# Optimization experiments

Hardware: AMD Instinct MI355X
Metric: run time of the kernel (lower is better)

Reference implementation:

```python
import jax, jax.numpy as jnp
import numpy as np

N_USERS = 100000
N_ITEMS = 50000
N = N_USERS + N_ITEMS
NNZ = 2400000
D = 64
L = 3
B = 16384


def setup_inputs() -> dict:
    key = jax.random.key(0)
    ks = jax.random.split(key, 12)
    return {
        "user_emb": jax.random.normal(ks[0], (N_USERS, D), jnp.float32) * 0.1,
        "item_emb": jax.random.normal(ks[1], (N_ITEMS, D), jnp.float32) * 0.1,
        "W_gc": jax.random.normal(ks[2], (L, D, D), jnp.float32) * 0.1,
        "b_gc": jax.random.normal(ks[3], (L, 1, D), jnp.float32) * 0.1,
        "W_bi": jax.random.normal(ks[4], (L, D, D), jnp.float32) * 0.1,
        "b_bi": jax.random.normal(ks[5], (L, 1, D), jnp.float32) * 0.1,
        "adj_vals": jax.random.uniform(ks[6], (NNZ,), jnp.float32) * (1.0 / 16.0),
        "adj_rows": jax.random.randint(ks[7], (NNZ,), 0, N, jnp.int32),
        "adj_cols": jax.random.randint(ks[8], (NNZ,), 0, N, jnp.int32),
        "u": jax.random.randint(ks[9], (B,), 0, N_USERS, jnp.int32),
        "i": jax.random.randint(ks[10], (B,), 0, N_ITEMS, jnp.int32),
        "j": jax.random.randint(ks[11], (B,), 0, N_ITEMS, jnp.int32),
    }


def reference(user_emb, item_emb, W_gc, b_gc, W_bi, b_bi, adj_vals, adj_rows, adj_cols, u, i, j):
    n_users = user_emb.shape[0]
    n_nodes = n_users + item_emb.shape[0]
    ego = jnp.concatenate([user_emb, item_emb], axis=0)  # [N, D]
    all_emb = [ego]
    n_layers = W_gc.shape[0]
    for l in range(n_layers):
        # spmm: side = A_hat @ ego  (edge-list gather + weighted segment sum)
        gathered = ego[adj_cols] * adj_vals[:, None]            # [nnz, D]
        side = jax.ops.segment_sum(gathered, adj_rows, num_segments=n_nodes)  # [N, D]
        # graph-conv branch
        sum_emb = jax.nn.leaky_relu(side @ W_gc[l] + b_gc[l], 0.2)
        # bi-interaction branch
        bi_emb = jax.nn.leaky_relu((ego * side) @ W_bi[l] + b_bi[l], 0.2)
        ego = sum_emb + bi_emb
        # L2 normalize per node (F.normalize, eps=1e-12)
        norm = ego / jnp.maximum(jnp.linalg.norm(ego, axis=1, keepdims=True), 1e-12)
        all_emb.append(norm)
    final = jnp.concatenate(all_emb, axis=1)  # [N, D*(L+1)]
    u_g = final[u]
    i_g = final[n_users + i]
    j_g = final[n_users + j]
    return u_g, i_g, j_g
```

## Files before the change

kernel.cpp:

```cpp
#include <hip/hip_runtime.h>

#define DD 64
#define RB 256
#define RB_SHIFT 8
#define CAP 4608
#define NBLKA 512
#define NBLKA_SHIFT 9
#define BMAX 1024
#define COLM 0x3FFFF
#define OVFCAP 65536
#define WT_STRIDE 80
#define EMAX 4704

typedef __attribute__((ext_vector_type(8))) short bf16x8;
typedef __attribute__((ext_vector_type(4))) float f32x4;

static __device__ __forceinline__ float leaky(float x) {
    return x > 0.f ? x : 0.2f * x;
}

static __device__ __forceinline__ unsigned short f2bf(float f) {
    unsigned u = __float_as_uint(f);
    unsigned r = 0x7FFFu + ((u >> 16) & 1u);
    return (unsigned short)((u + r) >> 16);
}
#define BF_LO(w) __int_as_float((int)((w) << 16))
#define BF_HI(w) __int_as_float((int)((w) & 0xFFFF0000u))

static __device__ __forceinline__ bf16x8 pack8(float a, float b, float c, float d,
                                               float e, float f, float g, float h) {
    bf16x8 r;
    r[0] = (short)f2bf(a); r[1] = (short)f2bf(b); r[2] = (short)f2bf(c); r[3] = (short)f2bf(d);
    r[4] = (short)f2bf(e); r[5] = (short)f2bf(f); r[6] = (short)f2bf(g); r[7] = (short)f2bf(h);
    return r;
}

__global__ void concat_kernel(const float4* __restrict__ ue, const float4* __restrict__ ie,
                              float4* __restrict__ ego, ushort4* __restrict__ egob,
                              int n_user4, int total4) {
    int idx = blockIdx.x * blockDim.x + threadIdx.x;
    if (idx >= total4) return;
    float4 v = (idx < n_user4) ? ue[idx] : ie[idx - n_user4];
    ego[idx] = v;
    ushort4 b;
    b.x = f2bf(v.x); b.y = f2bf(v.y); b.z = f2bf(v.z); b.w = f2bf(v.w);
    egob[idx] = b;
}

__global__ void bhist_kernel(const int* __restrict__ rows, int* __restrict__ counts_t, int nnz,
                             int nbuckets) {
    __shared__ int h[BMAX];
    int tid = threadIdx.x, blk = blockIdx.x;
    for (int i = tid; i < nbuckets; i += 256) h[i] = 0;
    __syncthreads();
    int chunk = (nnz + NBLKA - 1) / NBLKA;
    int lo = blk * chunk, hi = min(nnz, lo + chunk);
    for (int e = lo + tid; e < hi; e += 256) atomicAdd(&h[rows[e] >> RB_SHIFT], 1);
    __syncthreads();
    for (int i = tid; i < nbuckets; i += 256) counts_t[blk * nbuckets + i] = h[i];
}

__global__ void scan1_kernel(const int* __restrict__ counts_t, int* __restrict__ offsets,
                             int* __restrict__ blocksums, int flat, int nbuckets) {
    __shared__ int tmp[1024];
    int t = threadIdx.x;
    int g = blockIdx.x * 1024 + t;
    int x = 0;
    if (g < flat) {
        int i = g >> NBLKA_SHIFT, blk = g & (NBLKA - 1);
        x = counts_t[blk * nbuckets + i];
    }
    tmp[t] = x;
    __syncthreads();
    for (int off = 1; off < 1024; off <<= 1) {
        int y = (t >= off) ? tmp[t - off] : 0;
        __syncthreads();
        tmp[t] += y;
        __syncthreads();
    }
    if (g < flat) offsets[g + 1] = tmp[t];
    if (t == 1023) blocksums[blockIdx.x] = tmp[t];
    if (g == 0) offsets[0] = 0;
}

__global__ void scan2_kernel(int* blocksums, int nb) {
    __shared__ int tmp[1024];
    int t = threadIdx.x;
    int v = (t < nb) ? blocksums[t] : 0;
    tmp[t] = v;
    __syncthreads();
    for (int off = 1; off < 1024; off <<= 1) {
        int y = (t >= off) ? tmp[t - off] : 0;
        __syncthreads();
        tmp[t] += y;
        __syncthreads();
    }
    if (t < nb) blocksums[t] = tmp[t] - v;
}

__global__ void scan3_kernel(int* __restrict__ offsets, const int* __restrict__ blocksums,
                             int n) {
    int g = blockIdx.x * 1024 + threadIdx.x;
    if (g < n) offsets[g + 1] += blocksums[blockIdx.x];
}

__global__ void __launch_bounds__(256) bscatter_kernel(
    const int* __restrict__ rows, const int* __restrict__ cols,
    const float* __restrict__ vals, const int* __restrict__ offsets,
    int2* __restrict__ csr_cv, int nnz, int nbuckets) {
    __shared__ int hist[BMAX];
    __shared__ int lbase[BMAX];
    __shared__ int cur[BMAX];
    __shared__ int gcur[BMAX];
    __shared__ int tsum[256];
    __shared__ int2 buf[EMAX];
    __shared__ int dst[EMAX];
    int tid = threadIdx.x, blk = blockIdx.x;
    int chunk = (nnz + NBLKA - 1) / NBLKA;
    int lo = blk * chunk, hi = min(nnz, lo + chunk);
    for (int i = tid; i < BMAX; i += 256)
        gcur[i] = (i < nbuckets) ? offsets[i * NBLKA + blk] : 0;
    for (int sub = lo; sub < hi; sub += EMAX) {
        int scount = min(EMAX, hi - sub);
        for (int i = tid; i < BMAX; i += 256) hist[i] = 0;
        __syncthreads();
        for (int e = sub + tid; e < sub + scount; e += 256)
            atomicAdd(&hist[rows[e] >> RB_SHIFT], 1);
        __syncthreads();
        int loc[4];
        int s = 0;
        int bi = tid * 4;
#pragma unroll
        for (int j = 0; j < 4; ++j) { loc[j] = s; s += hist[bi + j]; }
        tsum[tid] = s;
        __syncthreads();
        for (int off = 1; off < 256; off <<= 1) {
            int v = (tid >= off) ? tsum[tid - off] : 0;
            __syncthreads();
            tsum[tid] += v;
            __syncthreads();
        }
        int excl = tid ? tsum[tid - 1] : 0;
#pragma unroll
        for (int j = 0; j < 4; ++j) {
            lbase[bi + j] = excl + loc[j];
            cur[bi + j] = excl + loc[j];
        }
        __syncthreads();
        for (int e = sub + tid; e < sub + scount; e += 256) {
            int r = rows[e];
            int b = r >> RB_SHIFT;
            int p = atomicAdd(&cur[b], 1);
            int2 cv;
            cv.x = ((r & (RB - 1)) << 18) | cols[e];
            cv.y = __float_as_int(vals[e]);
            buf[p] = cv;
            dst[p] = gcur[b] + (p - lbase[b]);
        }
        __syncthreads();
        for (int k = tid; k < scount; k += 256) csr_cv[dst[k]] = buf[k];
        __syncthreads();
        for (int i = tid; i < BMAX; i += 256) gcur[i] += hist[i];
        __syncthreads();
    }
}

__global__ void __launch_bounds__(256) sort_kernel(
    const int* __restrict__ offsets, const int2* __restrict__ csr_cv,
    int2* __restrict__ sorted_cv, int* __restrict__ rowoff_g,
    int4* __restrict__ ovf, int* __restrict__ ovf_cnt, int nnz, int nbuckets) {
    __shared__ int2 sorted[CAP];
    __shared__ int hist[RB];
    __shared__ int rowoff[RB + 1];
    __shared__ int cur[RB];
    int tid = threadIdx.x;
    int b = blockIdx.x;
    int s = offsets[b * NBLKA];
    int e = offsets[(b + 1) * NBLKA];
    int m = min(e - s, CAP);

    hist[tid] = 0;
    __syncthreads();
    for (int k = s + tid; k < s + m; k += 256)
        atomicAdd(&hist[((unsigned)csr_cv[k].x) >> 18], 1);
    __syncthreads();
    for (int off = 1; off < RB; off <<= 1) {
        int v = (tid >= off) ? hist[tid - off] : 0;
        __syncthreads();
        hist[tid] += v;
        __syncthreads();
    }
    rowoff[tid + 1] = hist[tid];
    if (tid == 0) rowoff[0] = 0;
    __syncthreads();
    cur[tid] = rowoff[tid];
    __syncthreads();
    for (int k = s + tid; k < s + m; k += 256) {
        int2 cv = csr_cv[k];
        int p = atomicAdd(&cur[((unsigned)cv.x) >> 18], 1);
        sorted[p] = cv;
    }
    __syncthreads();
    for (int k = tid; k < m; k += 256) sorted_cv[s + k] = sorted[k];
    rowoff_g[b * RB + tid] = s + rowoff[tid];
    if (b == 0 && tid == 0) rowoff_g[nbuckets * RB] = nnz;
    for (int k = s + CAP + tid; k < e; k += 256) {
        int2 cv = csr_cv[k];
        int p = atomicAdd(ovf_cnt, 1);
        if (p < OVFCAP) {
            int4 o;
            o.x = b * RB + (int)(((unsigned)cv.x) >> 18);
            o.y = cv.x & COLM;
            o.z = cv.y;
            o.w = 0;
            ovf[p] = o;
        }
    }
}

__global__ void spmm_csr_kernel(const uint4* __restrict__ egob4,
                                const int* __restrict__ rowoff,
                                const int2* __restrict__ sorted_cv,
                                float4* __restrict__ side4, int n) {
    int wid = (blockIdx.x * blockDim.x + threadIdx.x) >> 6;
    int lane = threadIdx.x & 63;
    int sub = lane >> 3, l8 = lane & 7;
    int row = wid * 8 + sub;
    if (row >= n) return;
    int s = rowoff[row], e = rowoff[row + 1];
    float acc[8] = {0.f, 0.f, 0.f, 0.f, 0.f, 0.f, 0.f, 0.f};
    int k = s;
    for (; k + 4 <= e; k += 4) {
        int2 c0 = sorted_cv[k];
        int2 c1 = sorted_cv[k + 1];
        int2 c2 = sorted_cv[k + 2];
        int2 c3 = sorted_cv[k + 3];
        uint4 g0 = egob4[(c0.x & COLM) * 8 + l8];
        uint4 g1 = egob4[(c1.x & COLM) * 8 + l8];
        uint4 g2 = egob4[(c2.x & COLM) * 8 + l8];
        uint4 g3 = egob4[(c3.x & COLM) * 8 + l8];
        float v0 = __int_as_float(c0.y), v1 = __int_as_float(c1.y);
        float v2 = __int_as_float(c2.y), v3 = __int_as_float(c3.y);
        acc[0] += v0 * BF_LO(g0.x); acc[1] += v0 * BF_HI(g0.x);
        acc[2] += v0 * BF_LO(g0.y); acc[3] += v0 * BF_HI(g0.y);
        acc[4] += v0 * BF_LO(g0.z); acc[5] += v0 * BF_HI(g0.z);
        acc[6] += v0 * BF_LO(g0.w); acc[7] += v0 * BF_HI(g0.w);
        acc[0] += v1 * BF_LO(g1.x); acc[1] += v1 * BF_HI(g1.x);
        acc[2] += v1 * BF_LO(g1.y); acc[3] += v1 * BF_HI(g1.y);
        acc[4] += v1 * BF_LO(g1.z); acc[5] += v1 * BF_HI(g1.z);
        acc[6] += v1 * BF_LO(g1.w); acc[7] += v1 * BF_HI(g1.w);
        acc[0] += v2 * BF_LO(g2.x); acc[1] += v2 * BF_HI(g2.x);
        acc[2] += v2 * BF_LO(g2.y); acc[3] += v2 * BF_HI(g2.y);
        acc[4] += v2 * BF_LO(g2.z); acc[5] += v2 * BF_HI(g2.z);
        acc[6] += v2 * BF_LO(g2.w); acc[7] += v2 * BF_HI(g2.w);
        acc[0] += v3 * BF_LO(g3.x); acc[1] += v3 * BF_HI(g3.x);
        acc[2] += v3 * BF_LO(g3.y); acc[3] += v3 * BF_HI(g3.y);
        acc[4] += v3 * BF_LO(g3.z); acc[5] += v3 * BF_HI(g3.z);
        acc[6] += v3 * BF_LO(g3.w); acc[7] += v3 * BF_HI(g3.w);
    }
    for (; k < e; ++k) {
        int2 cv = sorted_cv[k];
        uint4 g = egob4[(cv.x & COLM) * 8 + l8];
        float v = __int_as_float(cv.y);
        acc[0] += v * BF_LO(g.x); acc[1] += v * BF_HI(g.x);
        acc[2] += v * BF_LO(g.y); acc[3] += v * BF_HI(g.y);
        acc[4] += v * BF_LO(g.z); acc[5] += v * BF_HI(g.z);
        acc[6] += v * BF_LO(g.w); acc[7] += v * BF_HI(g.w);
    }
    float4 o0 = {acc[0], acc[1], acc[2], acc[3]};
    float4 o1 = {acc[4], acc[5], acc[6], acc[7]};
    side4[row * 16 + l8 * 2] = o0;
    side4[row * 16 + l8 * 2 + 1] = o1;
}

__global__ void ovf_fix_kernel(const int4* __restrict__ ovf, const int* __restrict__ ovf_cnt,
                               const float* __restrict__ ego, float* __restrict__ side) {
    int total = min(*ovf_cnt, OVFCAP);
    for (int i = blockIdx.x * blockDim.x + threadIdx.x; i < total * DD;
         i += gridDim.x * blockDim.x) {
        int e = i >> 6, d = i & 63;
        int4 o = ovf[e];
        atomicAdd(&side[o.x * DD + d], __int_as_float(o.z) * ego[o.y * DD + d]);
    }
}

__global__ void __launch_bounds__(256) transform_kernel(
    const float* __restrict__ side, float* __restrict__ ego, ushort* __restrict__ egob,
    const float* __restrict__ Wgc, const float* __restrict__ bgc,
    const float* __restrict__ Wbi, const float* __restrict__ bbi, int n) {
    __shared__ __align__(16) ushort sWg[DD * WT_STRIDE];
    __shared__ __align__(16) ushort sWb[DD * WT_STRIDE];
    int tid = threadIdx.x;
    for (int idx = tid; idx < DD * DD; idx += 256) {
        int k = idx >> 6, c = idx & 63;
        sWg[c * WT_STRIDE + k] = f2bf(Wgc[idx]);
        sWb[c * WT_STRIDE + k] = f2bf(Wbi[idx]);
    }
    __syncthreads();

    int wave = tid >> 6, lane = tid & 63;
    int ntiles = (n + 15) >> 4;
    int tile = blockIdx.x * 4 + wave;
    if (tile >= ntiles) return;
    int base = tile * 16;
    int m = lane & 15, quad = lane >> 4;
    int row = base + m;
    if (row >= n) row = n - 1;

    const float4* srow = (const float4*)(side + (size_t)row * DD);
    const float4* erow = (const float4*)(ego + (size_t)row * DD);
    float4 s0 = srow[quad * 2], s1 = srow[quad * 2 + 1];
    float4 s2 = srow[8 + quad * 2], s3 = srow[8 + quad * 2 + 1];
    float4 e0 = erow[quad * 2], e1 = erow[quad * 2 + 1];
    float4 e2 = erow[8 + quad * 2], e3 = erow[8 + quad * 2 + 1];

    bf16x8 aS_lo = pack8(s0.x, s0.y, s0.z, s0.w, s1.x, s1.y, s1.z, s1.w);
    bf16x8 aS_hi = pack8(s2.x, s2.y, s2.z, s2.w, s3.x, s3.y, s3.z, s3.w);
    bf16x8 aP_lo = pack8(e0.x * s0.x, e0.y * s0.y, e0.z * s0.z, e0.w * s0.w,
                         e1.x * s1.x, e1.y * s1.y, e1.z * s1.z, e1.w * s1.w);
    bf16x8 aP_hi = pack8(e2.x * s2.x, e2.y * s2.y, e2.z * s2.z, e2.w * s2.w,
                         e3.x * s3.x, e3.y * s3.y, e3.z * s3.z, e3.w * s3.w);

    f32x4 accG[4], accB[4];
#pragma unroll
    for (int ct = 0; ct < 4; ++ct) {
        accG[ct] = (f32x4){0.f, 0.f, 0.f, 0.f};
        accB[ct] = (f32x4){0.f, 0.f, 0.f, 0.f};
    }
#pragma unroll
    for (int ct = 0; ct < 4; ++ct) {
        int col = ct * 16 + m;
        bf16x8 bg_lo = *(const bf16x8*)&sWg[col * WT_STRIDE + quad * 8];
        bf16x8 bg_hi = *(const bf16x8*)&sWg[col * WT_STRIDE + 32 + quad * 8];
        bf16x8 bb_lo = *(const bf16x8*)&sWb[col * WT_STRIDE + quad * 8];
        bf16x8 bb_hi = *(const bf16x8*)&sWb[col * WT_STRIDE + 32 + quad * 8];
        accG[ct] = __builtin_amdgcn_mfma_f32_16x16x32_bf16(aS_lo, bg_lo, accG[ct], 0, 0, 0);
        accG[ct] = __builtin_amdgcn_mfma_f32_16x16x32_bf16(aS_hi, bg_hi, accG[ct], 0, 0, 0);
        accB[ct] = __builtin_amdgcn_mfma_f32_16x16x32_bf16(aP_lo, bb_lo, accB[ct], 0, 0, 0);
        accB[ct] = __builtin_amdgcn_mfma_f32_16x16x32_bf16(aP_hi, bb_hi, accB[ct], 0, 0, 0);
    }

#pragma unroll
    for (int ct = 0; ct < 4; ++ct) {
        int col = ct * 16 + m;
        float bg = bgc[col], bb = bbi[col];
#pragma unroll
        for (int r = 0; r < 4; ++r) {
            int node = base + quad * 4 + r;
            if (node < n) {
                float o = leaky(accG[ct][r] + bg) + leaky(accB[ct][r] + bb);
                ego[(size_t)node * DD + col] = o;
                egob[(size_t)node * DD + col] = f2bf(o);
            }
        }
    }
}

__global__ void gather_kernel(const float* __restrict__ ego, const int* __restrict__ u,
                              const int* __restrict__ ii, const int* __restrict__ jj,
                              float* __restrict__ out, int layer, int B, int n_users,
                              int normalize) {
    int wid = (blockIdx.x * blockDim.x + threadIdx.x) >> 6;
    int lane = threadIdx.x & 63;
    if (wid >= 3 * B) return;
    int arr = wid / B;
    int b = wid - arr * B;
    int node = (arr == 0) ? u[b] : ((arr == 1) ? n_users + ii[b] : n_users + jj[b]);
    float v = ego[node * DD + lane];
    if (normalize) {
        float ss = v * v;
#pragma unroll
        for (int m = 32; m; m >>= 1) ss += __shfl_xor(ss, m, 64);
        v /= fmaxf(sqrtf(ss), 1e-12f);
    }
    out[wid * 256 + layer * DD + lane] = v;
}

extern "C" void kernel_launch(void* const* d_in, const int* in_sizes, int n_in,
                              void* d_out, int out_size, void* d_ws, size_t ws_size,
                              hipStream_t stream) {
    const float* user_emb = (const float*)d_in[0];
    const float* item_emb = (const float*)d_in[1];
    const float* W_gc = (const float*)d_in[2];
    const float* b_gc = (const float*)d_in[3];
    const float* W_bi = (const float*)d_in[4];
    const float* b_bi = (const float*)d_in[5];
    const float* adj_vals = (const float*)d_in[6];
    const int* adj_rows = (const int*)d_in[7];
    const int* adj_cols = (const int*)d_in[8];
    const int* u = (const int*)d_in[9];
    const int* ii = (const int*)d_in[10];
    const int* jj = (const int*)d_in[11];
    float* out = (float*)d_out;

    const int D = DD;
    int n_users = in_sizes[0] / D;
    int n_items = in_sizes[1] / D;
    int n = n_users + n_items;
    int nnz = in_sizes[6];
    int B = in_sizes[9];
    int L = in_sizes[2] / (D * D);

    int nbuckets = (n + RB - 1) / RB;
    int flat = nbuckets * NBLKA;

    char* ws = (char*)d_ws;
    auto alloc = [&](size_t bytes) {
        char* p = ws;
        ws += (bytes + 255) & ~(size_t)255;
        return p;
    };
    float* ego = (float*)alloc((size_t)n * D * 4);
    ushort* egob = (ushort*)alloc((size_t)n * D * 2);
    float* side = (float*)alloc((size_t)n * D * 4);
    int* counts_t = (int*)alloc((size_t)flat * 4);
    int* offsets = (int*)alloc((size_t)(flat + 1) * 4);
    int* blocksums = (int*)alloc(4096);
    int2* csr_cv = (int2*)alloc((size_t)nnz * 8);
    int2* sorted_cv = (int2*)alloc((size_t)nnz * 8);
    int* rowoff = (int*)alloc((size_t)(nbuckets * RB + 1) * 4);
    int4* ovf = (int4*)alloc((size_t)OVFCAP * 16);
    int* ovf_cnt = (int*)alloc(256);

    int total4 = n * D / 4, nu4 = n_users * D / 4;
    concat_kernel<<<(total4 + 255) / 256, 256, 0, stream>>>(
        (const float4*)user_emb, (const float4*)item_emb, (float4*)ego, (ushort4*)egob,
        nu4, total4);

    int grows = 3 * B;
    gather_kernel<<<(grows + 3) / 4, 256, 0, stream>>>(ego, u, ii, jj, out, 0, B, n_users, 0);

    hipMemsetAsync(ovf_cnt, 0, 4, stream);
    bhist_kernel<<<NBLKA, 256, 0, stream>>>(adj_rows, counts_t, nnz, nbuckets);
    int nblk1 = (flat + 1023) / 1024;
    scan1_kernel<<<nblk1, 1024, 0, stream>>>(counts_t, offsets, blocksums, flat, nbuckets);
    scan2_kernel<<<1, 1024, 0, stream>>>(blocksums, nblk1);
    scan3_kernel<<<nblk1, 1024, 0, stream>>>(offsets, blocksums, flat);
    bscatter_kernel<<<NBLKA, 256, 0, stream>>>(adj_rows, adj_cols, adj_vals, offsets, csr_cv,
                                               nnz, nbuckets);
    sort_kernel<<<nbuckets, 256, 0, stream>>>(offsets, csr_cv, sorted_cv, rowoff, ovf, ovf_cnt,
                                              nnz, nbuckets);

    int spmm_waves = (n + 7) / 8;
    int spmm_blocks = (spmm_waves * 64 + 255) / 256;
    int ntiles = (n + 15) / 16;
    for (int l = 0; l < L; ++l) {
        spmm_csr_kernel<<<spmm_blocks, 256, 0, stream>>>(
            (const uint4*)egob, rowoff, sorted_cv, (float4*)side, n);
        ovf_fix_kernel<<<64, 256, 0, stream>>>(ovf, ovf_cnt, ego, side);
        transform_kernel<<<(ntiles + 3) / 4, 256, 0, stream>>>(
            side, ego, egob, W_gc + (size_t)l * D * D, b_gc + (size_t)l * D,
            W_bi + (size_t)l * D * D, b_bi + (size_t)l * D, n);
        gather_kernel<<<(grows + 3) / 4, 256, 0, stream>>>(ego, u, ii, jj, out, l + 1, B,
                                                           n_users, 1);
    }
}
```

Baseline: 496.2 us.

## Fuse SpMM and dense transform per layer, drop overflow path

Merges the CSR SpMM and the dense transform into one kernel per layer. Each block aggregates 64 rows into shared memory and then applies the bf16 MFMA transform, with ego and egob double-buffered across layers. This removes the full side-matrix write and read plus two launches per layer. The sort kernel now writes buckets larger than CAP directly to global memory instead of using the overflow list and atomic fixup kernel. The cost is extra shared memory per block, which may lower occupancy for the gather-bound SpMM phase.

```diff
diff --git a/kernel.cpp b/kernel.cpp
--- a/kernel.cpp
+++ b/kernel.cpp
@@ -8,9 +8,9 @@
 #define NBLKA_SHIFT 9
 #define BMAX 1024
 #define COLM 0x3FFFF
-#define OVFCAP 65536
 #define WT_STRIDE 80
 #define EMAX 4704
+#define SPAD 68
 
 typedef __attribute__((ext_vector_type(8))) short bf16x8;
 typedef __attribute__((ext_vector_type(4))) float f32x4;
@@ -167,8 +167,7 @@
 
 __global__ void __launch_bounds__(256) sort_kernel(
     const int* __restrict__ offsets, const int2* __restrict__ csr_cv,
-    int2* __restrict__ sorted_cv, int* __restrict__ rowoff_g,
-    int4* __restrict__ ovf, int* __restrict__ ovf_cnt, int nnz, int nbuckets) {
+    int2* __restrict__ sorted_cv, int* __restrict__ rowoff_g, int nnz, int nbuckets) {
     __shared__ int2 sorted[CAP];
     __shared__ int hist[RB];
     __shared__ int rowoff[RB + 1];
@@ -177,11 +176,11 @@
     int b = blockIdx.x;
     int s = offsets[b * NBLKA];
     int e = offsets[(b + 1) * NBLKA];
-    int m = min(e - s, CAP);
+    int m = e - s;
 
     hist[tid] = 0;
     __syncthreads();
-    for (int k = s + tid; k < s + m; k += 256)
+    for (int k = s + tid; k < e; k += 256)
         atomicAdd(&hist[((unsigned)csr_cv[k].x) >> 18], 1);
     __syncthreads();
     for (int off = 1; off < RB; off <<= 1) {
@@ -195,99 +194,32 @@
     __syncthreads();
     cur[tid] = rowoff[tid];
     __syncthreads();
-    for (int k = s + tid; k < s + m; k += 256) {
-        int2 cv = csr_cv[k];
-        int p = atomicAdd(&cur[((unsigned)cv.x) >> 18], 1);
-        sorted[p] = cv;
-    }
-    __syncthreads();
-    for (int k = tid; k < m; k += 256) sorted_cv[s + k] = sorted[k];
+    if (m <= CAP) {
+        for (int k = s + tid; k < e; k += 256) {
+            int2 cv = csr_cv[k];
+            int p = atomicAdd(&cur[((unsigned)cv.x) >> 18], 1);
+            sorted[p] = cv;
+        }
+        __syncthreads();
+        for (int k = tid; k < m; k += 256) sorted_cv[s + k] = sorted[k];
+    } else {
+        for (int k = s + tid; k < e; k += 256) {
+            int2 cv = csr_cv[k];
+            int p = atomicAdd(&cur[((unsigned)cv.x) >> 18], 1);
+            sorted_cv[s + p] = cv;
+        }
+    }
     rowoff_g[b * RB + tid] = s + rowoff[tid];
     if (b == 0 && tid == 0) rowoff_g[nbuckets * RB] = nnz;
-    for (int k = s + CAP + tid; k < e; k += 256) {
-        int2 cv = csr_cv[k];
-        int p = atomicAdd(ovf_cnt, 1);
-        if (p < OVFCAP) {
-            int4 o;
-            o.x = b * RB + (int)(((unsigned)cv.x) >> 18);
-            o.y = cv.x & COLM;
-            o.z = cv.y;
-            o.w = 0;
-            ovf[p] = o;
-        }
-    }
-}
-
-__global__ void spmm_csr_kernel(const uint4* __restrict__ egob4,
-                                const int* __restrict__ rowoff,
-                                const int2* __restrict__ sorted_cv,
-                                float4* __restrict__ side4, int n) {
-    int wid = (blockIdx.x * blockDim.x + threadIdx.x) >> 6;
-    int lane = threadIdx.x & 63;
-    int sub = lane >> 3, l8 = lane & 7;
-    int row = wid * 8 + sub;
-    if (row >= n) return;
-    int s = rowoff[row], e = rowoff[row + 1];
-    float acc[8] = {0.f, 0.f, 0.f, 0.f, 0.f, 0.f, 0.f, 0.f};
-    int k = s;
-    for (; k + 4 <= e; k += 4) {
-        int2 c0 = sorted_cv[k];
-        int2 c1 = sorted_cv[k + 1];
-        int2 c2 = sorted_cv[k + 2];
-        int2 c3 = sorted_cv[k + 3];
-        uint4 g0 = egob4[(c0.x & COLM) * 8 + l8];
-        uint4 g1 = egob4[(c1.x & COLM) * 8 + l8];
-        uint4 g2 = egob4[(c2.x & COLM) * 8 + l8];
-        uint4 g3 = egob4[(c3.x & COLM) * 8 + l8];
-        float v0 = __int_as_float(c0.y), v1 = __int_as_float(c1.y);
-        float v2 = __int_as_float(c2.y), v3 = __int_as_float(c3.y);
-        acc[0] += v0 * BF_LO(g0.x); acc[1] += v0 * BF_HI(g0.x);
-        acc[2] += v0 * BF_LO(g0.y); acc[3] += v0 * BF_HI(g0.y);
-        acc[4] += v0 * BF_LO(g0.z); acc[5] += v0 * BF_HI(g0.z);
-        acc[6] += v0 * BF_LO(g0.w); acc[7] += v0 * BF_HI(g0.w);
-        acc[0] += v1 * BF_LO(g1.x); acc[1] += v1 * BF_HI(g1.x);
-        acc[2] += v1 * BF_LO(g1.y); acc[3] += v1 * BF_HI(g1.y);
-        acc[4] += v1 * BF_LO(g1.z); acc[5] += v1 * BF_HI(g1.z);
-        acc[6] += v1 * BF_LO(g1.w); acc[7] += v1 * BF_HI(g1.w);
-        acc[0] += v2 * BF_LO(g2.x); acc[1] += v2 * BF_HI(g2.x);
-        acc[2] += v2 * BF_LO(g2.y); acc[3] += v2 * BF_HI(g2.y);
-        acc[4] += v2 * BF_LO(g2.z); acc[5] += v2 * BF_HI(g2.z);
-        acc[6] += v2 * BF_LO(g2.w); acc[7] += v2 * BF_HI(g2.w);
-        acc[0] += v3 * BF_LO(g3.x); acc[1] += v3 * BF_HI(g3.x);
-        acc[2] += v3 * BF_LO(g3.y); acc[3] += v3 * BF_HI(g3.y);
-        acc[4] += v3 * BF_LO(g3.z); acc[5] += v3 * BF_HI(g3.z);
-        acc[6] += v3 * BF_LO(g3.w); acc[7] += v3 * BF_HI(g3.w);
-    }
-    for (; k < e; ++k) {
-        int2 cv = sorted_cv[k];
-        uint4 g = egob4[(cv.x & COLM) * 8 + l8];
-        float v = __int_as_float(cv.y);
-        acc[0] += v * BF_LO(g.x); acc[1] += v * BF_HI(g.x);
-        acc[2] += v * BF_LO(g.y); acc[3] += v * BF_HI(g.y);
-        acc[4] += v * BF_LO(g.z); acc[5] += v * BF_HI(g.z);
-        acc[6] += v * BF_LO(g.w); acc[7] += v * BF_HI(g.w);
-    }
-    float4 o0 = {acc[0], acc[1], acc[2], acc[3]};
-    float4 o1 = {acc[4], acc[5], acc[6], acc[7]};
-    side4[row * 16 + l8 * 2] = o0;
-    side4[row * 16 + l8 * 2 + 1] = o1;
-}
-
-__global__ void ovf_fix_kernel(const int4* __restrict__ ovf, const int* __restrict__ ovf_cnt,
-                               const float* __restrict__ ego, float* __restrict__ side) {
-    int total = min(*ovf_cnt, OVFCAP);
-    for (int i = blockIdx.x * blockDim.x + threadIdx.x; i < total * DD;
-         i += gridDim.x * blockDim.x) {
-        int e = i >> 6, d = i & 63;
-        int4 o = ovf[e];
-        atomicAdd(&side[o.x * DD + d], __int_as_float(o.z) * ego[o.y * DD + d]);
-    }
-}
-
-__global__ void __launch_bounds__(256) transform_kernel(
-    const float* __restrict__ side, float* __restrict__ ego, ushort* __restrict__ egob,
+}
+
+__global__ void __launch_bounds__(256) fused_layer_kernel(
+    const uint4* __restrict__ egob_old, const float* __restrict__ ego_old,
+    float* __restrict__ ego_new, ushort* __restrict__ egob_new,
+    const int* __restrict__ rowoff, const int2* __restrict__ sorted_cv,
     const float* __restrict__ Wgc, const float* __restrict__ bgc,
     const float* __restrict__ Wbi, const float* __restrict__ bbi, int n) {
+    __shared__ __align__(16) float sideL[64 * SPAD];
     __shared__ __align__(16) ushort sWg[DD * WT_STRIDE];
     __shared__ __align__(16) ushort sWb[DD * WT_STRIDE];
     int tid = threadIdx.x;
@@ -296,21 +228,73 @@
         sWg[c * WT_STRIDE + k] = f2bf(Wgc[idx]);
         sWb[c * WT_STRIDE + k] = f2bf(Wbi[idx]);
     }
-    __syncthreads();
-
+    int base64 = blockIdx.x * 64;
     int wave = tid >> 6, lane = tid & 63;
-    int ntiles = (n + 15) >> 4;
-    int tile = blockIdx.x * 4 + wave;
-    if (tile >= ntiles) return;
-    int base = tile * 16;
+    int sub = lane >> 3, l8 = lane & 7;
+
+#pragma unroll
+    for (int pass = 0; pass < 2; ++pass) {
+        int lr = pass * 32 + wave * 8 + sub;
+        int row = base64 + lr;
+        float acc[8] = {0.f, 0.f, 0.f, 0.f, 0.f, 0.f, 0.f, 0.f};
+        if (row < n) {
+            int s = rowoff[row], e = rowoff[row + 1];
+            int k = s;
+            for (; k + 4 <= e; k += 4) {
+                int2 c0 = sorted_cv[k];
+                int2 c1 = sorted_cv[k + 1];
+                int2 c2 = sorted_cv[k + 2];
+                int2 c3 = sorted_cv[k + 3];
+                uint4 g0 = egob_old[(c0.x & COLM) * 8 + l8];
+                uint4 g1 = egob_old[(c1.x & COLM) * 8 + l8];
+                uint4 g2 = egob_old[(c2.x & COLM) * 8 + l8];
+                uint4 g3 = egob_old[(c3.x & COLM) * 8 + l8];
+                float v0 = __int_as_float(c0.y), v1 = __int_as_float(c1.y);
+                float v2 = __int_as_float(c2.y), v3 = __int_as_float(c3.y);
+                acc[0] += v0 * BF_LO(g0.x); acc[1] += v0 * BF_HI(g0.x);
+                acc[2] += v0 * BF_LO(g0.y); acc[3] += v0 * BF_HI(g0.y);
+                acc[4] += v0 * BF_LO(g0.z); acc[5] += v0 * BF_HI(g0.z);
+                acc[6] += v0 * BF_LO(g0.w); acc[7] += v0 * BF_HI(g0.w);
+                acc[0] += v1 * BF_LO(g1.x); acc[1] += v1 * BF_HI(g1.x);
+                acc[2] += v1 * BF_LO(g1.y); acc[3] += v1 * BF_HI(g1.y);
+                acc[4] += v1 * BF_LO(g1.z); acc[5] += v1 * BF_HI(g1.z);
+                acc[6] += v1 * BF_LO(g1.w); acc[7] += v1 * BF_HI(g1.w);
+                acc[0] += v2 * BF_LO(g2.x); acc[1] += v2 * BF_HI(g2.x);
+                acc[2] += v2 * BF_LO(g2.y); acc[3] += v2 * BF_HI(g2.y);
+                acc[4] += v2 * BF_LO(g2.z); acc[5] += v2 * BF_HI(g2.z);
+                acc[6] += v2 * BF_LO(g2.w); acc[7] += v2 * BF_HI(g2.w);
+                acc[0] += v3 * BF_LO(g3.x); acc[1] += v3 * BF_HI(g3.x);
+                acc[2] += v3 * BF_LO(g3.y); acc[3] += v3 * BF_HI(g3.y);
+                acc[4] += v3 * BF_LO(g3.z); acc[5] += v3 * BF_HI(g3.z);
+                acc[6] += v3 * BF_LO(g3.w); acc[7] += v3 * BF_HI(g3.w);
+            }
+            for (; k < e; ++k) {
+                int2 cv = sorted_cv[k];
+                uint4 g = egob_old[(cv.x & COLM) * 8 + l8];
+                float v = __int_as_float(cv.y);
+                acc[0] += v * BF_LO(g.x); acc[1] += v * BF_HI(g.x);
+                acc[2] += v * BF_LO(g.y); acc[3] += v * BF_HI(g.y);
+                acc[4] += v * BF_LO(g.z); acc[5] += v * BF_HI(g.z);
+                acc[6] += v * BF_LO(g.w); acc[7] += v * BF_HI(g.w);
+            }
+        }
+        float4 o0 = {acc[0], acc[1], acc[2], acc[3]};
+        float4 o1 = {acc[4], acc[5], acc[6], acc[7]};
+        *(float4*)&sideL[lr * SPAD + l8 * 8] = o0;
+        *(float4*)&sideL[lr * SPAD + l8 * 8 + 4] = o1;
+    }
+    __syncthreads();
+
     int m = lane & 15, quad = lane >> 4;
-    int row = base + m;
-    if (row >= n) row = n - 1;
-
-    const float4* srow = (const float4*)(side + (size_t)row * DD);
-    const float4* erow = (const float4*)(ego + (size_t)row * DD);
-    float4 s0 = srow[quad * 2], s1 = srow[quad * 2 + 1];
-    float4 s2 = srow[8 + quad * 2], s3 = srow[8 + quad * 2 + 1];
+    int lr = wave * 16 + m;
+    int base = base64 + wave * 16;
+    int rowc = min(base64 + lr, n - 1);
+
+    float4 s0 = *(const float4*)&sideL[lr * SPAD + quad * 8];
+    float4 s1 = *(const float4*)&sideL[lr * SPAD + quad * 8 + 4];
+    float4 s2 = *(const float4*)&sideL[lr * SPAD + 32 + quad * 8];
+    float4 s3 = *(const float4*)&sideL[lr * SPAD + 32 + quad * 8 + 4];
+    const float4* erow = (const float4*)(ego_old + (size_t)rowc * DD);
     float4 e0 = erow[quad * 2], e1 = erow[quad * 2 + 1];
     float4 e2 = erow[8 + quad * 2], e3 = erow[8 + quad * 2 + 1];
 
@@ -349,8 +333,8 @@
             int node = base + quad * 4 + r;
             if (node < n) {
                 float o = leaky(accG[ct][r] + bg) + leaky(accB[ct][r] + bb);
-                ego[(size_t)node * DD + col] = o;
-                egob[(size_t)node * DD + col] = f2bf(o);
+                ego_new[(size_t)node * DD + col] = o;
+                egob_new[(size_t)node * DD + col] = f2bf(o);
             }
         }
     }
@@ -410,27 +394,25 @@
         ws += (bytes + 255) & ~(size_t)255;
         return p;
     };
-    float* ego = (float*)alloc((size_t)n * D * 4);
-    ushort* egob = (ushort*)alloc((size_t)n * D * 2);
-    float* side = (float*)alloc((size_t)n * D * 4);
+    float* ego_a = (float*)alloc((size_t)n * D * 4);
+    float* ego_b = (float*)alloc((size_t)n * D * 4);
+    ushort* egob_a = (ushort*)alloc((size_t)n * D * 2);
+    ushort* egob_b = (ushort*)alloc((size_t)n * D * 2);
     int* counts_t = (int*)alloc((size_t)flat * 4);
     int* offsets = (int*)alloc((size_t)(flat + 1) * 4);
     int* blocksums = (int*)alloc(4096);
     int2* csr_cv = (int2*)alloc((size_t)nnz * 8);
     int2* sorted_cv = (int2*)alloc((size_t)nnz * 8);
     int* rowoff = (int*)alloc((size_t)(nbuckets * RB + 1) * 4);
-    int4* ovf = (int4*)alloc((size_t)OVFCAP * 16);
-    int* ovf_cnt = (int*)alloc(256);
 
     int total4 = n * D / 4, nu4 = n_users * D / 4;
     concat_kernel<<<(total4 + 255) / 256, 256, 0, stream>>>(
-        (const float4*)user_emb, (const float4*)item_emb, (float4*)ego, (ushort4*)egob,
+        (const float4*)user_emb, (const float4*)item_emb, (float4*)ego_a, (ushort4*)egob_a,
         nu4, total4);
 
     int grows = 3 * B;
-    gather_kernel<<<(grows + 3) / 4, 256, 0, stream>>>(ego, u, ii, jj, out, 0, B, n_users, 0);
-
-    hipMemsetAsync(ovf_cnt, 0, 4, stream);
+    gather_kernel<<<(grows + 3) / 4, 256, 0, stream>>>(ego_a, u, ii, jj, out, 0, B, n_users, 0);
+
     bhist_kernel<<<NBLKA, 256, 0, stream>>>(adj_rows, counts_t, nnz, nbuckets);
     int nblk1 = (flat + 1023) / 1024;
     scan1_kernel<<<nblk1, 1024, 0, stream>>>(counts_t, offsets, blocksums, flat, nbuckets);
@@ -438,20 +420,19 @@
     scan3_kernel<<<nblk1, 1024, 0, stream>>>(offsets, blocksums, flat);
     bscatter_kernel<<<NBLKA, 256, 0, stream>>>(adj_rows, adj_cols, adj_vals, offsets, csr_cv,
                                                nnz, nbuckets);
-    sort_kernel<<<nbuckets, 256, 0, stream>>>(offsets, csr_cv, sorted_cv, rowoff, ovf, ovf_cnt,
-                                              nnz, nbuckets);
-
-    int spmm_waves = (n + 7) / 8;
-    int spmm_blocks = (spmm_waves * 64 + 255) / 256;
-    int ntiles = (n + 15) / 16;
+    sort_kernel<<<nbuckets, 256, 0, stream>>>(offsets, csr_cv, sorted_cv, rowoff, nnz, nbuckets);
+
+    float* eo = ego_a; ushort* ebo = egob_a;
+    float* en = ego_b; ushort* ebn = egob_b;
+    int fblocks = (n + 63) / 64;
     for (int l = 0; l < L; ++l) {
-        spmm_csr_kernel<<<spmm_blocks, 256, 0, stream>>>(
-            (const uint4*)egob, rowoff, sorted_cv, (float4*)side, n);
-        ovf_fix_kernel<<<64, 256, 0, stream>>>(ovf, ovf_cnt, ego, side);
-        transform_kernel<<<(ntiles + 3) / 4, 256, 0, stream>>>(
-            side, ego, egob, W_gc + (size_t)l * D * D, b_gc + (size_t)l * D,
+        fused_layer_kernel<<<fblocks, 256, 0, stream>>>(
+            (const uint4*)ebo, eo, en, ebn, rowoff, sorted_cv,
+            W_gc + (size_t)l * D * D, b_gc + (size_t)l * D,
             W_bi + (size_t)l * D * D, b_bi + (size_t)l * D, n);
-        gather_kernel<<<(grows + 3) / 4, 256, 0, stream>>>(ego, u, ii, jj, out, l + 1, B,
+        gather_kernel<<<(grows + 3) / 4, 256, 0, stream>>>(en, u, ii, jj, out, l + 1, B,
                                                            n_users, 1);
-    }
-}
+        float* tf = eo; eo = en; en = tf;
+        ushort* tb = ebo; ebo = ebn; ebn = tb;
+    }
+}
```

Result: faster. 479.6 us (-3.3%).
